# Kernel tuning notes

Measured on AMD Instinct MI355X. Metric: run time of the kernel, lower is better.

The kernel has to match this reference:

```python
import jax, jax.numpy as jnp
import numpy as np

D_MODEL = 1024
N_HEADS = 16
HEAD_DIM = D_MODEL // N_HEADS
B, T = 2, 2048


def setup_inputs() -> dict:
    key = jax.random.key(0)
    ks = jax.random.split(key, 6)
    x = jax.random.normal(ks[0], (B, T, D_MODEL), dtype=jnp.float32)
    tgt_key_padding_mask = jnp.zeros((B, T), dtype=bool)
    scale = 0.02
    Wq = jax.random.normal(ks[1], (D_MODEL, D_MODEL), dtype=jnp.float32) * scale
    Wk = jax.random.normal(ks[2], (D_MODEL, D_MODEL), dtype=jnp.float32) * scale
    Wv = jax.random.normal(ks[3], (D_MODEL, D_MODEL), dtype=jnp.float32) * scale
    Wo = jax.random.normal(ks[4], (D_MODEL, D_MODEL), dtype=jnp.float32) * scale
    return {"x": x, "tgt_key_padding_mask": tgt_key_padding_mask,
            "Wq": Wq, "Wk": Wk, "Wv": Wv, "Wo": Wo}


def reference(x, tgt_key_padding_mask, Wq, Wk, Wv, Wo):
    # Eval-mode (dropout disabled) masked causal MHA, faithful to torch module.
    b, t, c = x.shape
    h, d = N_HEADS, HEAD_DIM
    # nn.Linear(bias=False): y = x @ W.T
    Q = (x @ Wq.T).reshape(b, t, h, d).transpose(0, 2, 1, 3)  # [B,H,T,d]
    K = (x @ Wk.T).reshape(b, t, h, d).transpose(0, 2, 1, 3)
    V = (x @ Wv.T).reshape(b, t, h, d).transpose(0, 2, 1, 3)
    scores = jnp.einsum('bhqd,bhkd->bhqk', Q, K) / jnp.sqrt(jnp.float32(d))
    # causal mask: True above the diagonal -> -inf
    cmask = jnp.triu(jnp.ones((t, t), dtype=bool), k=1)  # [T,T]
    neg_inf = jnp.float32(-jnp.inf)
    scores = jnp.where(cmask[None, None, :, :], neg_inf, scores)
    # key padding mask: [B,T] True=PAD, broadcast over query dim
    pmask = tgt_key_padding_mask[:, None, None, :]  # [B,1,1,T]
    scores = jnp.where(pmask, neg_inf, scores)
    attn = jax.nn.softmax(scores, axis=-1)
    out = jnp.einsum('bhqk,bhkd->bhqd', attn, V)  # [B,H,T,d]
    out = out.transpose(0, 2, 1, 3).reshape(b, t, c)
    out = out @ Wo.T
    return out
```

## Files before the change

kernel.cpp:

```cpp
#include <hip/hip_runtime.h>
#include <hip/hip_bf16.h>
#include <stdint.h>

#define D_MODEL 1024
#define NHEADS  16
#define HDIM    64
#define BB      2
#define TT      2048
#define MROWS   (BB*TT)
#define GK      1024

typedef __bf16 bf16_8 __attribute__((ext_vector_type(8)));
typedef __bf16 bf16_4 __attribute__((ext_vector_type(4)));
typedef float  f32x4  __attribute__((ext_vector_type(4)));
typedef unsigned short u16;

__device__ __forceinline__ u16 f2bf(float f) {
    union { float f; uint32_t u; } c; c.f = f;
    uint32_t u = c.u;
    uint32_t r = (u + 0x7FFFu + ((u >> 16) & 1u)) >> 16;
    return (u16)r;
}
__device__ __forceinline__ uint32_t pk2bf(float a, float b) {
    return (uint32_t)f2bf(a) | ((uint32_t)f2bf(b) << 16);
}

__device__ __forceinline__ void gload16(const void* g, void* l) {
    __builtin_amdgcn_global_load_lds(
        (const __attribute__((address_space(1))) unsigned int*)g,
        (__attribute__((address_space(3))) unsigned int*)l,
        16, 0, 0);
}

__global__ __launch_bounds__(256) void cvtk(
    const float* __restrict__ x,  const float* __restrict__ wq,
    const float* __restrict__ wk, const float* __restrict__ wv,
    const float* __restrict__ wo, const unsigned char* __restrict__ mk,
    u16* __restrict__ xb,  u16* __restrict__ wqb, u16* __restrict__ wkb,
    u16* __restrict__ wvb, u16* __restrict__ wob, uint32_t* __restrict__ pmb)
{
    int z = blockIdx.y;
    if (z == 5) {
        int gi = blockIdx.x*256 + threadIdx.x;
        if (gi < BB*TT/32) {
            uint32_t wv = 0;
            #pragma unroll
            for (int j = 0; j < 32; ++j)
                wv |= (mk[gi*32 + j] ? 1u : 0u) << j;
            pmb[gi] = wv;
        }
        return;
    }
    const float* in; u16* out; int n4;
    switch (z) {
        case 0: in = x;  out = xb;  n4 = MROWS*D_MODEL/4; break;
        case 1: in = wq; out = wqb; n4 = D_MODEL*D_MODEL/4; break;
        case 2: in = wk; out = wkb; n4 = D_MODEL*D_MODEL/4; break;
        case 3: in = wv; out = wvb; n4 = D_MODEL*D_MODEL/4; break;
        default: in = wo; out = wob; n4 = D_MODEL*D_MODEL/4; break;
    }
    for (int i = blockIdx.x*256 + threadIdx.x; i < n4; i += 1024*256) {
        float4 v = ((const float4*)in)[i];
        uint2 pk;
        pk.x = pk2bf(v.x, v.y);
        pk.y = pk2bf(v.z, v.w);
        ((uint2*)out)[i] = pk;
    }
}

__global__ __launch_bounds__(256) void gemm_qkv(
    const u16* __restrict__ xb,
    const u16* __restrict__ wqb, const u16* __restrict__ wkb, const u16* __restrict__ wvb,
    u16* __restrict__ Qb, u16* __restrict__ Kb, u16* __restrict__ VTb)
{
    __shared__ u16 As[128*64];
    __shared__ u16 Bs[3][64*64];
    const int tid  = threadIdx.x;
    const int lane = tid & 63, w = tid >> 6;
    const int g = lane >> 4, lr = lane & 15;
    const int xcd = blockIdx.x & 7, q_ = blockIdx.x >> 3;
    const int bn = q_ & 15, bm = (q_ >> 4)*8 + xcd;
    const int m0 = bm * 128, n0 = bn * 64;
    const u16* Wz[3] = { wqb, wkb, wvb };

    f32x4 acc[3][2][4];
    #pragma unroll
    for (int z = 0; z < 3; ++z)
        #pragma unroll
        for (int i = 0; i < 2; ++i)
            #pragma unroll
            for (int j = 0; j < 4; ++j)
                acc[z][i][j] = f32x4{0.f, 0.f, 0.f, 0.f};

    for (int kt = 0; kt < 16; ++kt) {
        int k0 = kt*64;
        #pragma unroll
        for (int r = 0; r < 4; ++r) {
            int o   = r*256 + tid;
            int row = o >> 3;
            int lc  = (o & 7) ^ (row & 7);
            gload16(xb + (size_t)(m0+row)*GK + k0 + lc*8,
                    (char*)As + (size_t)(r*256 + w*64)*16);
        }
        #pragma unroll
        for (int z = 0; z < 3; ++z)
            #pragma unroll
            for (int r = 0; r < 2; ++r) {
                int o   = r*256 + tid;
                int row = o >> 3;
                int lc  = (o & 7) ^ (row & 7);
                gload16(Wz[z] + (size_t)(n0+row)*GK + k0 + lc*8,
                        (char*)&Bs[z][0] + (size_t)(r*256 + w*64)*16);
            }
        __syncthreads();
        #pragma unroll
        for (int ks = 0; ks < 2; ++ks) {
            bf16_8 af[2];
            #pragma unroll
            for (int mt = 0; mt < 2; ++mt) {
                int row = w*32 + mt*16 + lr;
                int ch  = (ks*4 + g) ^ (row & 7);
                af[mt] = *(const bf16_8*)((const char*)As + row*128 + ch*16);
            }
            #pragma unroll
            for (int z = 0; z < 3; ++z) {
                bf16_8 bfr[4];
                #pragma unroll
                for (int nt = 0; nt < 4; ++nt) {
                    int row = nt*16 + lr;
                    int ch  = (ks*4 + g) ^ (row & 7);
                    bfr[nt] = *(const bf16_8*)((const char*)&Bs[z][0] + row*128 + ch*16);
                }
                #pragma unroll
                for (int mt = 0; mt < 2; ++mt)
                    #pragma unroll
                    for (int nt = 0; nt < 4; ++nt) {
                        if (z == 2)
                            acc[2][mt][nt] = __builtin_amdgcn_mfma_f32_16x16x32_bf16(
                                bfr[nt], af[mt], acc[2][mt][nt], 0, 0, 0);
                        else
                            acc[z][mt][nt] = __builtin_amdgcn_mfma_f32_16x16x32_bf16(
                                af[mt], bfr[nt], acc[z][mt][nt], 0, 0, 0);
                    }
            }
        }
        __syncthreads();
    }

    #pragma unroll
    for (int mt = 0; mt < 2; ++mt)
        #pragma unroll
        for (int nt = 0; nt < 4; ++nt)
            #pragma unroll
            for (int r = 0; r < 4; ++r) {
                int row = m0 + w*32 + mt*16 + g*4 + r;
                int col = n0 + nt*16 + lr;
                int b = row >> 11, t = row & (TT-1);
                int h = col >> 6,  d = col & 63;
                size_t qi = (((size_t)(b*NHEADS + h)*TT + t)*HDIM + d);
                Qb[qi] = f2bf(acc[0][mt][nt][r] * 0.18033688f);
                Kb[qi] = f2bf(acc[1][mt][nt][r]);
                int nrow = n0 + nt*16 + g*4 + r;
                int mcol = m0 + w*32 + mt*16 + lr;
                int hv = nrow >> 6,  dv = nrow & 63;
                int bv = mcol >> 11, tv = mcol & (TT-1);
                VTb[(((size_t)(bv*NHEADS + hv)*HDIM + dv)*TT + tv)] = f2bf(acc[2][mt][nt][r]);
            }
}

__global__ __launch_bounds__(256) void gemm_out(
    const u16* __restrict__ AOb, const u16* __restrict__ wob, float* __restrict__ out)
{
    __shared__ u16 As[128*64];
    __shared__ u16 Bs[64*64];
    const int tid  = threadIdx.x;
    const int lane = tid & 63, w = tid >> 6;
    const int g = lane >> 4, lr = lane & 15;
    const int xcd = blockIdx.x & 7, q_ = blockIdx.x >> 3;
    const int bn = q_ & 15, bm = (q_ >> 4)*8 + xcd;
    const int m0 = bm * 128, n0 = bn * 64;

    f32x4 acc[2][4];
    #pragma unroll
    for (int i = 0; i < 2; ++i)
        #pragma unroll
        for (int j = 0; j < 4; ++j)
            acc[i][j] = f32x4{0.f, 0.f, 0.f, 0.f};

    for (int kt = 0; kt < 16; ++kt) {
        int k0 = kt*64;
        #pragma unroll
        for (int r = 0; r < 4; ++r) {
            int o   = r*256 + tid;
            int row = o >> 3;
            int lc  = (o & 7) ^ (row & 7);
            gload16(AOb + (size_t)(m0+row)*GK + k0 + lc*8,
                    (char*)As + (size_t)(r*256 + w*64)*16);
        }
        #pragma unroll
        for (int r = 0; r < 2; ++r) {
            int o   = r*256 + tid;
            int row = o >> 3;
            int lc  = (o & 7) ^ (row & 7);
            gload16(wob + (size_t)(n0+row)*GK + k0 + lc*8,
                    (char*)Bs + (size_t)(r*256 + w*64)*16);
        }
        __syncthreads();
        #pragma unroll
        for (int ks = 0; ks < 2; ++ks) {
            bf16_8 af[2], bfr[4];
            #pragma unroll
            for (int mt = 0; mt < 2; ++mt) {
                int row = w*32 + mt*16 + lr;
                int ch  = (ks*4 + g) ^ (row & 7);
                af[mt] = *(const bf16_8*)((const char*)As + row*128 + ch*16);
            }
            #pragma unroll
            for (int nt = 0; nt < 4; ++nt) {
                int row = nt*16 + lr;
                int ch  = (ks*4 + g) ^ (row & 7);
                bfr[nt] = *(const bf16_8*)((const char*)Bs + row*128 + ch*16);
            }
            #pragma unroll
            for (int mt = 0; mt < 2; ++mt)
                #pragma unroll
                for (int nt = 0; nt < 4; ++nt)
                    acc[mt][nt] = __builtin_amdgcn_mfma_f32_16x16x32_bf16(
                        af[mt], bfr[nt], acc[mt][nt], 0, 0, 0);
        }
        __syncthreads();
    }

    #pragma unroll
    for (int mt = 0; mt < 2; ++mt)
        #pragma unroll
        for (int nt = 0; nt < 4; ++nt)
            #pragma unroll
            for (int r = 0; r < 4; ++r) {
                int row = m0 + w*32 + mt*16 + g*4 + r;
                int col = n0 + nt*16 + lr;
                out[(size_t)row*D_MODEL + col] = acc[mt][nt][r];
            }
}

__global__ __launch_bounds__(512, 4) void attn_fwd(
    const u16* __restrict__ Qb, const u16* __restrict__ Kb,
    const u16* __restrict__ VTb, const uint32_t* __restrict__ pmb,
    u16* __restrict__ AO)
{
    __shared__ u16 Ks[3][64*64];
    __shared__ u16 Vs[2][64*64];
    __shared__ u16 Pl[8][1152];
    __shared__ uint32_t Ml[64];

    const int tid = threadIdx.x, lane = tid & 63, w = tid >> 6;
    const int g = lane >> 4, lr = lane & 15;
    const int bh = blockIdx.x, yb = blockIdx.y;
    const int p  = (yb < 8) ? yb : 23 - yb;
    const int b = bh >> 4, h = bh & 15;
    const int qtH = 31 - p;
    const bool heavy = (w < 4);
    const int qlo = heavy ? (qtH*64 + w*16) : (p*64 + (w-4)*16);
    const int ta  = heavy ? qtH : p;
    const int nt  = qtH + 1;

    const u16* Qh = Qb  + (size_t)bh*TT*HDIM;
    const u16* Kh = Kb  + (size_t)bh*TT*HDIM;
    const u16* Vh = VTb + (size_t)bh*HDIM*TT;
    char* Pw = (char*)&Pl[w][0];

    if (tid < 64) Ml[tid] = pmb[b*(TT/32) + tid];

    bf16_8 qf[2];
    #pragma unroll
    for (int dc = 0; dc < 2; ++dc)
        qf[dc] = *(const bf16_8*)(Qh + (size_t)(qlo+lr)*HDIM + dc*32 + g*8);

    f32x4 o[4];
    #pragma unroll
    for (int i = 0; i < 4; ++i) o[i] = f32x4{0.f, 0.f, 0.f, 0.f};
    float l_run = 0.f;

    auto STAGE_K = [&](int t, int buf) {
        int kv0 = t*64;
        int row = tid >> 3;
        int lc  = (tid & 7) ^ (row & 7);
        gload16(Kh + (size_t)(kv0+row)*HDIM + lc*8,
                (char*)&Ks[buf][0] + (size_t)(w*64)*16);
    };
    auto STAGE_V = [&](int t, int buf) {
        int kv0 = t*64;
        int row = tid >> 3;
        int lc  = (tid & 7) ^ (row & 7);
        gload16(Vh + (size_t)row*TT + kv0 + lc*8,
                (char*)&Vs[buf][0] + (size_t)(w*64)*16);
    };

    STAGE_K(0, 0);
    STAGE_V(0, 0);
    STAGE_K(1, 1);

    int kb = 0;
    for (int t = 0; t < nt; ++t) {
        if (t + 1 < nt) asm volatile("s_waitcnt vmcnt(1) lgkmcnt(0)" ::: "memory");
        else            asm volatile("s_waitcnt vmcnt(0) lgkmcnt(0)" ::: "memory");
        __builtin_amdgcn_s_barrier();
        if (t + 1 < nt) STAGE_V(t+1, (t+1) & 1);
        if (t + 2 < nt) { int nk = kb + 2; if (nk >= 3) nk -= 3; STAGE_K(t+2, nk); }

        if (t <= ta) {
            const int kv0 = t*64;
            const u16* Kc = &Ks[kb][0];
            const u16* Vc = &Vs[t & 1][0];

            f32x4 s[4];
            __builtin_amdgcn_s_setprio(1);
            #pragma unroll
            for (int kvb = 0; kvb < 4; ++kvb) {
                int row = kvb*16 + lr;
                int sw  = row & 7;
                bf16_8 k0 = *(const bf16_8*)(Kc + row*64 + ((g    ) ^ sw)*8);
                bf16_8 k1 = *(const bf16_8*)(Kc + row*64 + ((4 + g) ^ sw)*8);
                f32x4 z = f32x4{0.f, 0.f, 0.f, 0.f};
                z = __builtin_amdgcn_mfma_f32_16x16x32_bf16(k0, qf[0], z, 0, 0, 0);
                z = __builtin_amdgcn_mfma_f32_16x16x32_bf16(k1, qf[1], z, 0, 0, 0);
                s[kvb] = z;
            }
            __builtin_amdgcn_s_setprio(0);

            bf16_8 vf[4][2];
            #pragma unroll
            for (int dt = 0; dt < 4; ++dt)
                #pragma unroll
                for (int hh = 0; hh < 2; ++hh)
                    vf[dt][hh] = *(const bf16_8*)(Vc + (dt*16+lr)*64 + ((hh*4+g) ^ (lr&7))*8);

            uint64_t m64 = (uint64_t)Ml[2*t] | ((uint64_t)Ml[2*t+1] << 32);
            if (m64) {
                #pragma unroll
                for (int kvb = 0; kvb < 4; ++kvb) {
                    uint32_t nib = (uint32_t)(m64 >> (kvb*16 + 4*g)) & 0xFu;
                    #pragma unroll
                    for (int r = 0; r < 4; ++r)
                        if ((nib >> r) & 1) s[kvb][r] = -1e30f;
                }
            }
            if (t == ta) {
                int q = qlo + lr;
                #pragma unroll
                for (int kvb = 0; kvb < 4; ++kvb) {
                    int kvb0 = kv0 + kvb*16 + 4*g;
                    #pragma unroll
                    for (int r = 0; r < 4; ++r)
                        if (kvb0 + r > q) s[kvb][r] = -1e30f;
                }
            }

            #pragma unroll
            for (int kvb = 0; kvb < 4; ++kvb)
                #pragma unroll
                for (int r = 0; r < 4; ++r)
                    s[kvb][r] = __builtin_amdgcn_exp2f(fminf(s[kvb][r], 80.f));
            float p0 = (s[0][0] + s[0][1]) + (s[0][2] + s[0][3]);
            float p1 = (s[1][0] + s[1][1]) + (s[1][2] + s[1][3]);
            float p2 = (s[2][0] + s[2][1]) + (s[2][2] + s[2][3]);
            float p3 = (s[3][0] + s[3][1]) + (s[3][2] + s[3][3]);
            float ps = (p0 + p1) + (p2 + p3);
            ps += __shfl_xor(ps, 16);
            ps += __shfl_xor(ps, 32);
            l_run += ps;

            #pragma unroll
            for (int kvb = 0; kvb < 4; ++kvb) {
                bf16_4 pk;
                pk[0] = (__bf16)s[kvb][0]; pk[1] = (__bf16)s[kvb][1];
                pk[2] = (__bf16)s[kvb][2]; pk[3] = (__bf16)s[kvb][3];
                *(bf16_4*)(Pw + lr*144 + kvb*32 + g*8) = pk;
            }
            asm volatile("s_waitcnt lgkmcnt(0)" ::: "memory");
            __builtin_amdgcn_sched_barrier(0);

            __builtin_amdgcn_s_setprio(1);
            #pragma unroll
            for (int hh = 0; hh < 2; ++hh) {
                bf16_8 pa = *(const bf16_8*)(Pw + lr*144 + hh*64 + g*16);
                #pragma unroll
                for (int dt = 0; dt < 4; ++dt)
                    o[dt] = __builtin_amdgcn_mfma_f32_16x16x32_bf16(
                        vf[dt][hh], pa, o[dt], 0, 0, 0);
            }
            __builtin_amdgcn_s_setprio(0);
        }

        ++kb; if (kb == 3) kb = 0;
    }

    float linv = (l_run > 0.f) ? 1.f/l_run : 0.f;
    u16* ot = (u16*)Pw;
    #pragma unroll
    for (int dt = 0; dt < 4; ++dt)
        #pragma unroll
        for (int r = 0; r < 4; ++r)
            ot[(dt*16 + 4*g + r)*17 + lr] = f2bf(o[dt][r]*linv);
    asm volatile("s_waitcnt lgkmcnt(0)" ::: "memory");
    __builtin_amdgcn_sched_barrier(0);
    #pragma unroll
    for (int qq = 0; qq < 16; ++qq)
        AO[((size_t)(b*TT + qlo + qq))*D_MODEL + h*HDIM + lane] = ot[lane*17 + qq];
}

extern "C" void kernel_launch(void* const* d_in, const int* in_sizes, int n_in,
                              void* d_out, int out_size, void* d_ws, size_t ws_size,
                              hipStream_t stream)
{
    const float* x  = (const float*)d_in[0];
    const unsigned char* mask = (const unsigned char*)d_in[1];
    const float* Wq = (const float*)d_in[2];
    const float* Wk = (const float*)d_in[3];
    const float* Wv = (const float*)d_in[4];
    const float* Wo = (const float*)d_in[5];
    float* out = (float*)d_out;

    char* ws = (char*)d_ws;
    u16* xb  = (u16*)(ws + 0);
    u16* wqb = (u16*)(ws + 8388608);
    u16* wkb = (u16*)(ws + 10485760);
    u16* wvb = (u16*)(ws + 12582912);
    u16* wob = (u16*)(ws + 14680064);
    u16* Qb  = (u16*)(ws + 16777216);
    u16* Kb  = (u16*)(ws + 25165824);
    u16* VTb = (u16*)(ws + 33554432);
    uint32_t* pmb = (uint32_t*)(ws + 41943040);
    u16* AOb = xb;

    cvtk<<<dim3(1024, 6), 256, 0, stream>>>(x, Wq, Wk, Wv, Wo, mask,
                                            xb, wqb, wkb, wvb, wob, pmb);
    gemm_qkv<<<dim3(512), 256, 0, stream>>>(xb, wqb, wkb, wvb, Qb, Kb, VTb);
    attn_fwd<<<dim3(32, 16), 512, 0, stream>>>(Qb, Kb, VTb, pmb, AOb);
    gemm_out<<<dim3(512), 256, 0, stream>>>(AOb, wob, out);
}
```

Before: 98.79 us.

## Give each attention wave two 16-row query groups with 256-thread blocks

Halves the attention block from 8 to 4 waves. Each wave now handles 32 query rows as two 16-row groups, so every K tile and V fragment read from shared memory feeds twice as many MFMAs. K/V staging is split into two loads per thread, and the wait count is adjusted to match. The trade-offs are more registers per wave, fewer waves to hide latency, and per-group softmax and P round-trips that are serialized within a wave.

New measurement: 108.8 us. 10.1% more time.

```diff
diff --git a/kernel.cpp b/kernel.cpp
--- a/kernel.cpp
+++ b/kernel.cpp
@@ -243,14 +243,14 @@
             }
 }
 
-__global__ __launch_bounds__(512, 4) void attn_fwd(
+__global__ __launch_bounds__(256, 2) void attn_fwd(
     const u16* __restrict__ Qb, const u16* __restrict__ Kb,
     const u16* __restrict__ VTb, const uint32_t* __restrict__ pmb,
     u16* __restrict__ AO)
 {
     __shared__ u16 Ks[3][64*64];
     __shared__ u16 Vs[2][64*64];
-    __shared__ u16 Pl[8][1152];
+    __shared__ u16 Pl[4][1152];
     __shared__ uint32_t Ml[64];
 
     const int tid = threadIdx.x, lane = tid & 63, w = tid >> 6;
@@ -259,8 +259,8 @@
     const int p  = (yb < 8) ? yb : 23 - yb;
     const int b = bh >> 4, h = bh & 15;
     const int qtH = 31 - p;
-    const bool heavy = (w < 4);
-    const int qlo = heavy ? (qtH*64 + w*16) : (p*64 + (w-4)*16);
+    const bool heavy = (w < 2);
+    const int qlo0 = heavy ? (qtH*64 + w*32) : (p*64 + (w-2)*32);
     const int ta  = heavy ? qtH : p;
     const int nt  = qtH + 1;
 
@@ -271,29 +271,41 @@
 
     if (tid < 64) Ml[tid] = pmb[b*(TT/32) + tid];
 
-    bf16_8 qf[2];
-    #pragma unroll
-    for (int dc = 0; dc < 2; ++dc)
-        qf[dc] = *(const bf16_8*)(Qh + (size_t)(qlo+lr)*HDIM + dc*32 + g*8);
-
-    f32x4 o[4];
-    #pragma unroll
-    for (int i = 0; i < 4; ++i) o[i] = f32x4{0.f, 0.f, 0.f, 0.f};
-    float l_run = 0.f;
+    bf16_8 qf[2][2];
+    #pragma unroll
+    for (int qg = 0; qg < 2; ++qg)
+        #pragma unroll
+        for (int dc = 0; dc < 2; ++dc)
+            qf[qg][dc] = *(const bf16_8*)(Qh + (size_t)(qlo0+qg*16+lr)*HDIM + dc*32 + g*8);
+
+    f32x4 o[2][4];
+    #pragma unroll
+    for (int qg = 0; qg < 2; ++qg)
+        #pragma unroll
+        for (int i = 0; i < 4; ++i) o[qg][i] = f32x4{0.f, 0.f, 0.f, 0.f};
+    float l_run[2] = {0.f, 0.f};
 
     auto STAGE_K = [&](int t, int buf) {
         int kv0 = t*64;
-        int row = tid >> 3;
-        int lc  = (tid & 7) ^ (row & 7);
-        gload16(Kh + (size_t)(kv0+row)*HDIM + lc*8,
-                (char*)&Ks[buf][0] + (size_t)(w*64)*16);
+        #pragma unroll
+        for (int r = 0; r < 2; ++r) {
+            int o_  = r*256 + tid;
+            int row = o_ >> 3;
+            int lc  = (o_ & 7) ^ (row & 7);
+            gload16(Kh + (size_t)(kv0+row)*HDIM + lc*8,
+                    (char*)&Ks[buf][0] + (size_t)(r*256 + w*64)*16);
+        }
     };
     auto STAGE_V = [&](int t, int buf) {
         int kv0 = t*64;
-        int row = tid >> 3;
-        int lc  = (tid & 7) ^ (row & 7);
-        gload16(Vh + (size_t)row*TT + kv0 + lc*8,
-                (char*)&Vs[buf][0] + (size_t)(w*64)*16);
+        #pragma unroll
+        for (int r = 0; r < 2; ++r) {
+            int o_  = r*256 + tid;
+            int row = o_ >> 3;
+            int lc  = (o_ & 7) ^ (row & 7);
+            gload16(Vh + (size_t)row*TT + kv0 + lc*8,
+                    (char*)&Vs[buf][0] + (size_t)(r*256 + w*64)*16);
+        }
     };
 
     STAGE_K(0, 0);
@@ -302,7 +314,7 @@
 
     int kb = 0;
     for (int t = 0; t < nt; ++t) {
-        if (t + 1 < nt) asm volatile("s_waitcnt vmcnt(1) lgkmcnt(0)" ::: "memory");
+        if (t + 1 < nt) asm volatile("s_waitcnt vmcnt(2) lgkmcnt(0)" ::: "memory");
         else            asm volatile("s_waitcnt vmcnt(0) lgkmcnt(0)" ::: "memory");
         __builtin_amdgcn_s_barrier();
         if (t + 1 < nt) STAGE_V(t+1, (t+1) & 1);
@@ -313,7 +325,7 @@
             const u16* Kc = &Ks[kb][0];
             const u16* Vc = &Vs[t & 1][0];
 
-            f32x4 s[4];
+            f32x4 s[2][4];
             __builtin_amdgcn_s_setprio(1);
             #pragma unroll
             for (int kvb = 0; kvb < 4; ++kvb) {
@@ -321,10 +333,13 @@
                 int sw  = row & 7;
                 bf16_8 k0 = *(const bf16_8*)(Kc + row*64 + ((g    ) ^ sw)*8);
                 bf16_8 k1 = *(const bf16_8*)(Kc + row*64 + ((4 + g) ^ sw)*8);
-                f32x4 z = f32x4{0.f, 0.f, 0.f, 0.f};
-                z = __builtin_amdgcn_mfma_f32_16x16x32_bf16(k0, qf[0], z, 0, 0, 0);
-                z = __builtin_amdgcn_mfma_f32_16x16x32_bf16(k1, qf[1], z, 0, 0, 0);
-                s[kvb] = z;
+                #pragma unroll
+                for (int qg = 0; qg < 2; ++qg) {
+                    f32x4 z = f32x4{0.f, 0.f, 0.f, 0.f};
+                    z = __builtin_amdgcn_mfma_f32_16x16x32_bf16(k0, qf[qg][0], z, 0, 0, 0);
+                    z = __builtin_amdgcn_mfma_f32_16x16x32_bf16(k1, qf[qg][1], z, 0, 0, 0);
+                    s[qg][kvb] = z;
+                }
             }
             __builtin_amdgcn_s_setprio(0);
 
@@ -336,77 +351,86 @@
                     vf[dt][hh] = *(const bf16_8*)(Vc + (dt*16+lr)*64 + ((hh*4+g) ^ (lr&7))*8);
 
             uint64_t m64 = (uint64_t)Ml[2*t] | ((uint64_t)Ml[2*t+1] << 32);
-            if (m64) {
-                #pragma unroll
-                for (int kvb = 0; kvb < 4; ++kvb) {
-                    uint32_t nib = (uint32_t)(m64 >> (kvb*16 + 4*g)) & 0xFu;
+
+            #pragma unroll
+            for (int qg = 0; qg < 2; ++qg) {
+                if (m64) {
+                    #pragma unroll
+                    for (int kvb = 0; kvb < 4; ++kvb) {
+                        uint32_t nib = (uint32_t)(m64 >> (kvb*16 + 4*g)) & 0xFu;
+                        #pragma unroll
+                        for (int r = 0; r < 4; ++r)
+                            if ((nib >> r) & 1) s[qg][kvb][r] = -1e30f;
+                    }
+                }
+                if (t == ta) {
+                    int q = qlo0 + qg*16 + lr;
+                    #pragma unroll
+                    for (int kvb = 0; kvb < 4; ++kvb) {
+                        int kvb0 = kv0 + kvb*16 + 4*g;
+                        #pragma unroll
+                        for (int r = 0; r < 4; ++r)
+                            if (kvb0 + r > q) s[qg][kvb][r] = -1e30f;
+                    }
+                }
+                #pragma unroll
+                for (int kvb = 0; kvb < 4; ++kvb)
                     #pragma unroll
                     for (int r = 0; r < 4; ++r)
-                        if ((nib >> r) & 1) s[kvb][r] = -1e30f;
-                }
-            }
-            if (t == ta) {
-                int q = qlo + lr;
+                        s[qg][kvb][r] = __builtin_amdgcn_exp2f(fminf(s[qg][kvb][r], 80.f));
+                float p0 = (s[qg][0][0] + s[qg][0][1]) + (s[qg][0][2] + s[qg][0][3]);
+                float p1 = (s[qg][1][0] + s[qg][1][1]) + (s[qg][1][2] + s[qg][1][3]);
+                float p2 = (s[qg][2][0] + s[qg][2][1]) + (s[qg][2][2] + s[qg][2][3]);
+                float p3 = (s[qg][3][0] + s[qg][3][1]) + (s[qg][3][2] + s[qg][3][3]);
+                float ps = (p0 + p1) + (p2 + p3);
+                ps += __shfl_xor(ps, 16);
+                ps += __shfl_xor(ps, 32);
+                l_run[qg] += ps;
+
                 #pragma unroll
                 for (int kvb = 0; kvb < 4; ++kvb) {
-                    int kvb0 = kv0 + kvb*16 + 4*g;
+                    bf16_4 pk;
+                    pk[0] = (__bf16)s[qg][kvb][0]; pk[1] = (__bf16)s[qg][kvb][1];
+                    pk[2] = (__bf16)s[qg][kvb][2]; pk[3] = (__bf16)s[qg][kvb][3];
+                    *(bf16_4*)(Pw + lr*144 + kvb*32 + g*8) = pk;
+                }
+                asm volatile("s_waitcnt lgkmcnt(0)" ::: "memory");
+                __builtin_amdgcn_sched_barrier(0);
+
+                __builtin_amdgcn_s_setprio(1);
+                #pragma unroll
+                for (int hh = 0; hh < 2; ++hh) {
+                    bf16_8 pa = *(const bf16_8*)(Pw + lr*144 + hh*64 + g*16);
                     #pragma unroll
-                    for (int r = 0; r < 4; ++r)
-                        if (kvb0 + r > q) s[kvb][r] = -1e30f;
-                }
-            }
-
-            #pragma unroll
-            for (int kvb = 0; kvb < 4; ++kvb)
-                #pragma unroll
-                for (int r = 0; r < 4; ++r)
-                    s[kvb][r] = __builtin_amdgcn_exp2f(fminf(s[kvb][r], 80.f));
-            float p0 = (s[0][0] + s[0][1]) + (s[0][2] + s[0][3]);
-            float p1 = (s[1][0] + s[1][1]) + (s[1][2] + s[1][3]);
-            float p2 = (s[2][0] + s[2][1]) + (s[2][2] + s[2][3]);
-            float p3 = (s[3][0] + s[3][1]) + (s[3][2] + s[3][3]);
-            float ps = (p0 + p1) + (p2 + p3);
-            ps += __shfl_xor(ps, 16);
-            ps += __shfl_xor(ps, 32);
-            l_run += ps;
-
-            #pragma unroll
-            for (int kvb = 0; kvb < 4; ++kvb) {
-                bf16_4 pk;
-                pk[0] = (__bf16)s[kvb][0]; pk[1] = (__bf16)s[kvb][1];
-                pk[2] = (__bf16)s[kvb][2]; pk[3] = (__bf16)s[kvb][3];
-                *(bf16_4*)(Pw + lr*144 + kvb*32 + g*8) = pk;
-            }
-            asm volatile("s_waitcnt lgkmcnt(0)" ::: "memory");
-            __builtin_amdgcn_sched_barrier(0);
-
-            __builtin_amdgcn_s_setprio(1);
-            #pragma unroll
-            for (int hh = 0; hh < 2; ++hh) {
-                bf16_8 pa = *(const bf16_8*)(Pw + lr*144 + hh*64 + g*16);
-                #pragma unroll
-                for (int dt = 0; dt < 4; ++dt)
-                    o[dt] = __builtin_amdgcn_mfma_f32_16x16x32_bf16(
-                        vf[dt][hh], pa, o[dt], 0, 0, 0);
-            }
-            __builtin_amdgcn_s_setprio(0);
+                    for (int dt = 0; dt < 4; ++dt)
+                        o[qg][dt] = __builtin_amdgcn_mfma_f32_16x16x32_bf16(
+                            vf[dt][hh], pa, o[qg][dt], 0, 0, 0);
+                }
+                __builtin_amdgcn_s_setprio(0);
+            }
         }
 
         ++kb; if (kb == 3) kb = 0;
     }
 
-    float linv = (l_run > 0.f) ? 1.f/l_run : 0.f;
-    u16* ot = (u16*)Pw;
-    #pragma unroll
-    for (int dt = 0; dt < 4; ++dt)
-        #pragma unroll
-        for (int r = 0; r < 4; ++r)
-            ot[(dt*16 + 4*g + r)*17 + lr] = f2bf(o[dt][r]*linv);
-    asm volatile("s_waitcnt lgkmcnt(0)" ::: "memory");
-    __builtin_amdgcn_sched_barrier(0);
-    #pragma unroll
-    for (int qq = 0; qq < 16; ++qq)
-        AO[((size_t)(b*TT + qlo + qq))*D_MODEL + h*HDIM + lane] = ot[lane*17 + qq];
+    #pragma unroll
+    for (int qg = 0; qg < 2; ++qg) {
+        float linv = (l_run[qg] > 0.f) ? 1.f/l_run[qg] : 0.f;
+        u16* ot = (u16*)Pw;
+        #pragma unroll
+        for (int dt = 0; dt < 4; ++dt)
+            #pragma unroll
+            for (int r = 0; r < 4; ++r)
+                ot[(dt*16 + 4*g + r)*17 + lr] = f2bf(o[qg][dt][r]*linv);
+        asm volatile("s_waitcnt lgkmcnt(0)" ::: "memory");
+        __builtin_amdgcn_sched_barrier(0);
+        const int qlo = qlo0 + qg*16;
+        #pragma unroll
+        for (int qq = 0; qq < 16; ++qq)
+            AO[((size_t)(b*TT + qlo + qq))*D_MODEL + h*HDIM + lane] = ot[lane*17 + qq];
+        asm volatile("s_waitcnt lgkmcnt(0)" ::: "memory");
+        __builtin_amdgcn_sched_barrier(0);
+    }
 }
 
 extern "C" void kernel_launch(void* const* d_in, const int* in_sizes, int n_in,
@@ -436,6 +460,6 @@
     cvtk<<<dim3(1024, 6), 256, 0, stream>>>(x, Wq, Wk, Wv, Wo, mask,
                                             xb, wqb, wkb, wvb, wob, pmb);
     gemm_qkv<<<dim3(512), 256, 0, stream>>>(xb, wqb, wkb, wvb, Qb, Kb, VTb);
-    attn_fwd<<<dim3(32, 16), 512, 0, stream>>>(Qb, Kb, VTb, pmb, AOb);
+    attn_fwd<<<dim3(32, 16), 256, 0, stream>>>(Qb, Kb, VTb, pmb, AOb);
     gemm_out<<<dim3(512), 256, 0, stream>>>(AOb, wob, out);
 }
```
